# Kernel optimization log

Measured on AMD Instinct MI355X. Metric: run time of the kernel, lower is better.

Reference implementation:

```python
import jax, jax.numpy as jnp
import numpy as np

DIM = 256
HEADS = 8
WS = 7
MLP_HIDDEN = int(DIM * 2.0)
LN_EPS = 1e-5


def _ln(x, g, b):
    m = x.mean(-1, keepdims=True)
    v = ((x - m) ** 2).mean(-1, keepdims=True)
    return (x - m) / jnp.sqrt(v + LN_EPS) * g + b


def setup_inputs() -> dict:
    key = jax.random.key(0)
    ks = jax.random.split(key, 6)
    B, H, W, C = 32, 56, 56, DIM
    s = lambda k, shape: jax.random.normal(k, shape, jnp.float32) * 0.02
    return {
        "x": jax.random.normal(ks[0], (B, H * W, C), jnp.float32),
        "H": H,
        "W": W,
        "norm1_g": jnp.ones((C,), jnp.float32),
        "norm1_b": jnp.zeros((C,), jnp.float32),
        "in_proj_w": s(ks[1], (3 * C, C)),
        "in_proj_b": jnp.zeros((3 * C,), jnp.float32),
        "out_proj_w": s(ks[2], (C, C)),
        "out_proj_b": jnp.zeros((C,), jnp.float32),
        "norm2_g": jnp.ones((C,), jnp.float32),
        "norm2_b": jnp.zeros((C,), jnp.float32),
        "mlp_w1": s(ks[3], (MLP_HIDDEN, C)),
        "mlp_b1": jnp.zeros((MLP_HIDDEN,), jnp.float32),
        "mlp_w2": s(ks[4], (C, MLP_HIDDEN)),
        "mlp_b2": jnp.zeros((C,), jnp.float32),
    }


def reference(x, H, W, norm1_g, norm1_b, in_proj_w, in_proj_b, out_proj_w,
              out_proj_b, norm2_g, norm2_b, mlp_w1, mlp_b1, mlp_w2, mlp_b2):
    B, N, C = x.shape
    ws = WS
    shortcut = x

    h = _ln(x, norm1_g, norm1_b).reshape(B, H, W, C)  # channels-last (equiv. math)
    pad_h = (ws - H % ws) % ws
    pad_w = (ws - W % ws) % ws
    h = jnp.pad(h, ((0, 0), (0, pad_h), (0, pad_w), (0, 0)), mode="reflect")
    Hp, Wp = H + pad_h, W + pad_w
    nh, nw = Hp // ws, Wp // ws

    # window partition -> (B*nh*nw, ws*ws, C)
    h = h.reshape(B, nh, ws, nw, ws, C).transpose(0, 1, 3, 2, 4, 5)
    h = h.reshape(B * nh * nw, ws * ws, C)

    # torch nn.MultiheadAttention (batch_first), q=k=v=h
    hd = C // HEADS
    qkv = h @ in_proj_w.T + in_proj_b               # (Bw, L, 3C)
    q, k, v = jnp.split(qkv, 3, axis=-1)
    Bw, L, _ = q.shape
    q = q.reshape(Bw, L, HEADS, hd).transpose(0, 2, 1, 3)
    k = k.reshape(Bw, L, HEADS, hd).transpose(0, 2, 1, 3)
    v = v.reshape(Bw, L, HEADS, hd).transpose(0, 2, 1, 3)
    scores = jnp.einsum("bhqd,bhkd->bhqk", q, k) / jnp.sqrt(jnp.float32(hd))
    attn = jax.nn.softmax(scores, axis=-1)
    o = jnp.einsum("bhqk,bhkd->bhqd", attn, v)
    o = o.transpose(0, 2, 1, 3).reshape(Bw, L, C)
    o = o @ out_proj_w.T + out_proj_b

    # window merge, crop padding
    o = o.reshape(B, nh, nw, ws, ws, C).transpose(0, 1, 3, 2, 4, 5)
    o = o.reshape(B, Hp, Wp, C)[:, :H, :W, :].reshape(B, N, C)

    x = shortcut + o
    h2 = _ln(x, norm2_g, norm2_b)
    h2 = jax.nn.gelu(h2 @ mlp_w1.T + mlp_b1, approximate=False) @ mlp_w2.T + mlp_b2
    return x + h2
```

## Files before the change

### kernel.cpp

```cpp
#include <hip/hip_runtime.h>
#include <hip/hip_bf16.h>
#include <math.h>

#define NTOK 3136
#define C_ 256
#define HEADS_ 8
#define HD 32
#define WS_ 7
#define L_ 49
#define NWIN 2048
#define NWH 16384
#define M_ 100352
#define MP 131072
#define PLANE 33554432
#define MLPH 512

typedef __bf16 bf16x8 __attribute__((ext_vector_type(8)));
typedef float f32x4 __attribute__((ext_vector_type(4)));

#define VMWAIT(n) asm volatile("s_waitcnt vmcnt(" #n ")" ::: "memory")
#define LGKWAIT   asm volatile("s_waitcnt lgkmcnt(0)" ::: "memory")
#define SBAR      __builtin_amdgcn_s_barrier()

__device__ __forceinline__ unsigned short f2bf(float f) {
    union { float f; unsigned u; } v; v.f = f;
    unsigned r = v.u + 0x7fffu + ((v.u >> 16) & 1u);
    return (unsigned short)(r >> 16);
}
__device__ __forceinline__ float bf2f(unsigned short s) {
    union { unsigned u; float f; } v; v.u = ((unsigned)s) << 16;
    return v.f;
}

__device__ __forceinline__ int t2rr(int t) {
    int win = t / L_;
    int l   = t - win * L_;
    int b_  = win >> 6, wh = (win >> 3) & 7, ww = win & 7;
    int ld7 = l / WS_;
    int y   = wh * WS_ + ld7;
    int xc  = ww * WS_ + (l - ld7 * WS_);
    return b_ * NTOK + y * 56 + xc;
}

template <int NBN>
__device__ __forceinline__ void xcd_decode(int nb, int& bm, int& bn) {
    int h = blockIdx.x;
    int fid = (h & 7) * (nb >> 3) + (h >> 3);
    int bmi = fid / NBN;
    bm = bmi * 128;
    bn = (fid - bmi * NBN) * 128;
}

__global__ __launch_bounds__(256) void cvt_kernel(
    const float* __restrict__ in, unsigned short* __restrict__ out, int n)
{
    int i = blockIdx.x * 256 + threadIdx.x;
    if (i < n) out[i] = f2bf(in[i]);
}

__global__ __launch_bounds__(256) void ln_kernel(
    const float* __restrict__ x, const float* __restrict__ gamma,
    const float* __restrict__ beta, unsigned short* __restrict__ out)
{
    int wave = threadIdx.x >> 6;
    int lane = threadIdx.x & 63;
    int p = blockIdx.x * 4 + wave;
    int win = p >> 6, l = p & 63;
    if (l >= L_) {
        uint2 z; z.x = 0; z.y = 0;
        *(uint2*)(out + (size_t)p * C_ + lane * 4) = z;
        return;
    }
    int b_ = win >> 6, wh = (win >> 3) & 7, ww = win & 7;
    int ld7 = l / WS_;
    int y   = wh * WS_ + ld7;
    int xc  = ww * WS_ + (l - ld7 * WS_);
    int rr  = b_ * NTOK + y * 56 + xc;
    const float* row = x + (size_t)rr * C_;
    float4 v = *(const float4*)(row + lane * 4);
    float s  = v.x + v.y + v.z + v.w;
    float ss = v.x * v.x + v.y * v.y + v.z * v.z + v.w * v.w;
    #pragma unroll
    for (int m = 1; m < 64; m <<= 1) {
        s  += __shfl_xor(s, m, 64);
        ss += __shfl_xor(ss, m, 64);
    }
    float mean = s * (1.0f / C_);
    float var  = ss * (1.0f / C_) - mean * mean;
    float inv  = rsqrtf(var + 1e-5f);
    float4 gv = *(const float4*)(gamma + lane * 4);
    float4 bv = *(const float4*)(beta + lane * 4);
    unsigned short o[4];
    o[0] = f2bf((v.x - mean) * inv * gv.x + bv.x);
    o[1] = f2bf((v.y - mean) * inv * gv.y + bv.y);
    o[2] = f2bf((v.z - mean) * inv * gv.z + bv.z);
    o[3] = f2bf((v.w - mean) * inv * gv.w + bv.w);
    *(uint2*)(out + (size_t)p * C_ + lane * 4) = *(const uint2*)o;
}

#define GBK 32

__device__ __forceinline__ void gload_lds16(const void* g, void* l) {
    __builtin_amdgcn_global_load_lds(
        (const __attribute__((address_space(1))) unsigned*)g,
        (__attribute__((address_space(3))) unsigned*)l, 16, 0, 0);
}

#define TSS 136

__global__ __launch_bounds__(256) void mgemm_qkv(
    const unsigned short* __restrict__ A, const unsigned short* __restrict__ W,
    const float* __restrict__ bias, unsigned short* __restrict__ Qp,
    unsigned short* __restrict__ Kp, unsigned short* __restrict__ Vp)
{
    __shared__ __align__(16) unsigned short pool[16384];
    unsigned short* As0 = pool;
    unsigned short* As1 = pool + 4096;
    unsigned short* Bs0 = pool + 8192;
    unsigned short* Bs1 = pool + 12288;
    unsigned short* Ts  = pool;

    int tid  = threadIdx.x;
    int w    = tid >> 6;
    int lane = tid & 63;
    int wr = w >> 1, wc = w & 1;
    int bm, bn;
    xcd_decode<6>(gridDim.x, bm, bn);
    int srow = lane >> 2;
    int scol = ((lane & 3) ^ ((lane >> 3) & 3)) * 8;
    int c = lane & 15, hi = lane >> 4;
    int hs = (hi ^ ((c >> 1) & 3)) * 8;

    f32x4 acc[4][4] = {};

    auto stage = [&](unsigned short* asd, unsigned short* bsd, int k0) {
        #pragma unroll
        for (int i = 0; i < 2; ++i) {
            int ra = w * 32 + i * 16;
            gload_lds16(A + (size_t)(bm + ra + srow) * 256 + k0 + scol, asd + ra * GBK);
            gload_lds16(W + (size_t)(bn + ra + srow) * 256 + k0 + scol, bsd + ra * GBK);
        }
    };

    stage(As0, Bs0, 0);
    stage(As1, Bs1, GBK);
    VMWAIT(4); SBAR;
    #pragma unroll
    for (int t = 0; t < 8; ++t) {
        unsigned short* as = (t & 1) ? As1 : As0;
        unsigned short* bs = (t & 1) ? Bs1 : Bs0;
        bf16x8 af[4], bf[4];
        #pragma unroll
        for (int mi = 0; mi < 4; ++mi)
            af[mi] = *(const bf16x8*)&as[(wr * 64 + mi * 16 + c) * GBK + hs];
        #pragma unroll
        for (int ni = 0; ni < 4; ++ni)
            bf[ni] = *(const bf16x8*)&bs[(wc * 64 + ni * 16 + c) * GBK + hs];
        LGKWAIT; SBAR;
        if (t + 2 < 8) stage(as, bs, (t + 2) * GBK);
        #pragma unroll
        for (int mi = 0; mi < 4; ++mi)
            #pragma unroll
            for (int ni = 0; ni < 4; ++ni)
                acc[mi][ni] = __builtin_amdgcn_mfma_f32_16x16x32_bf16(
                    af[mi], bf[ni], acc[mi][ni], 0, 0, 0);
        if (t < 7) {
            if (t + 2 < 8) { VMWAIT(4); } else { VMWAIT(0); }
            SBAR;
        }
    }
    __syncthreads();

    int which  = bn >> 8;
    int bn_off = bn & 255;
    unsigned short* plane = (which == 0) ? Qp : (which == 1) ? Kp : Vp;

    #pragma unroll
    for (int ch = 0; ch < 2; ++ch) {
        if (wr == ch) {
            #pragma unroll
            for (int mi = 0; mi < 4; ++mi)
                #pragma unroll
                for (int ni = 0; ni < 4; ++ni) {
                    int colb = wc * 64 + ni * 16 + c;
                    float bv = bias[bn + colb];
                    #pragma unroll
                    for (int r = 0; r < 4; ++r)
                        Ts[(mi * 16 + hi * 4 + r) * TSS + colb] =
                            f2bf(acc[mi][ni][r] + bv);
                }
        }
        __syncthreads();
        int win = (bm >> 6) + ch;
        if (which < 2) {
            #pragma unroll
            for (int it = 0; it < 4; ++it) {
                int id = it * 256 + tid;
                int row = id >> 4, cx = (id & 15) * 8;
                if (row < L_) {
                    uint4 v = *(const uint4*)&Ts[row * TSS + cx];
                    *(uint4*)&plane[(size_t)win * 16384 + (size_t)row * 256 + bn_off + cx] = v;
                }
            }
        } else {
            #pragma unroll
            for (int it = 0; it < 4; ++it) {
                int id = it * 256 + tid;
                int kb = id >> 7, colloc = id & 127;
                union { unsigned short s[8]; uint4 v; } u;
                #pragma unroll
                for (int kj = 0; kj < 8; ++kj)
                    u.s[kj] = Ts[(kb * 8 + kj) * TSS + colloc];
                *(uint4*)&plane[(size_t)win * 16384 +
                                (size_t)(kb * 256 + bn_off + colloc) * 8] = u.v;
            }
        }
        __syncthreads();
    }
}

__global__ __launch_bounds__(256) void mgemm_g(
    const unsigned short* __restrict__ A, const unsigned short* __restrict__ W,
    const float* __restrict__ bias, unsigned short* __restrict__ outp)
{
    __shared__ __align__(16) unsigned short pool[16384];
    unsigned short* As0 = pool;
    unsigned short* As1 = pool + 4096;
    unsigned short* Bs0 = pool + 8192;
    unsigned short* Bs1 = pool + 12288;
    unsigned short* Ts  = pool;

    int tid  = threadIdx.x;
    int w    = tid >> 6;
    int lane = tid & 63;
    int wr = w >> 1, wc = w & 1;
    int bm, bn;
    xcd_decode<4>(gridDim.x, bm, bn);
    int srow = lane >> 2;
    int scol = ((lane & 3) ^ ((lane >> 3) & 3)) * 8;
    int c = lane & 15, hi = lane >> 4;
    int hs = (hi ^ ((c >> 1) & 3)) * 8;

    f32x4 acc[4][4] = {};

    auto stage = [&](unsigned short* asd, unsigned short* bsd, int k0) {
        #pragma unroll
        for (int i = 0; i < 2; ++i) {
            int ra = w * 32 + i * 16;
            gload_lds16(A + (size_t)(bm + ra + srow) * 256 + k0 + scol, asd + ra * GBK);
            gload_lds16(W + (size_t)(bn + ra + srow) * 256 + k0 + scol, bsd + ra * GBK);
        }
    };

    stage(As0, Bs0, 0);
    stage(As1, Bs1, GBK);
    VMWAIT(4); SBAR;
    #pragma unroll
    for (int t = 0; t < 8; ++t) {
        unsigned short* as = (t & 1) ? As1 : As0;
        unsigned short* bs = (t & 1) ? Bs1 : Bs0;
        bf16x8 af[4], bf[4];
        #pragma unroll
        for (int mi = 0; mi < 4; ++mi)
            af[mi] = *(const bf16x8*)&as[(wr * 64 + mi * 16 + c) * GBK + hs];
        #pragma unroll
        for (int ni = 0; ni < 4; ++ni)
            bf[ni] = *(const bf16x8*)&bs[(wc * 64 + ni * 16 + c) * GBK + hs];
        LGKWAIT; SBAR;
        if (t + 2 < 8) stage(as, bs, (t + 2) * GBK);
        #pragma unroll
        for (int mi = 0; mi < 4; ++mi)
            #pragma unroll
            for (int ni = 0; ni < 4; ++ni)
                acc[mi][ni] = __builtin_amdgcn_mfma_f32_16x16x32_bf16(
                    af[mi], bf[ni], acc[mi][ni], 0, 0, 0);
        if (t < 7) {
            if (t + 2 < 8) { VMWAIT(4); } else { VMWAIT(0); }
            SBAR;
        }
    }
    __syncthreads();

    #pragma unroll
    for (int ch = 0; ch < 2; ++ch) {
        if (wr == ch) {
            #pragma unroll
            for (int mi = 0; mi < 4; ++mi)
                #pragma unroll
                for (int ni = 0; ni < 4; ++ni) {
                    int colb = wc * 64 + ni * 16 + c;
                    float bv = bias[bn + colb];
                    #pragma unroll
                    for (int r = 0; r < 4; ++r) {
                        float v = acc[mi][ni][r] + bv;
                        float a = 1.5957691216f * (v + 0.044715f * v * v * v);
                        float g = v / (1.0f + __expf(-a));
                        Ts[(mi * 16 + hi * 4 + r) * TSS + colb] = f2bf(g);
                    }
                }
        }
        __syncthreads();
        #pragma unroll
        for (int it = 0; it < 4; ++it) {
            int id = it * 256 + tid;
            int row = id >> 4, cx = (id & 15) * 8;
            uint4 v = *(const uint4*)&Ts[row * TSS + cx];
            *(uint4*)&outp[(size_t)(bm + ch * 64 + row) * MLPH + bn + cx] = v;
        }
        __syncthreads();
    }
}

#define XS 260

__global__ __launch_bounds__(512) void mgemm_ln(
    const unsigned short* __restrict__ A, const unsigned short* __restrict__ W,
    const float* __restrict__ bias, const float* __restrict__ x,
    const float* __restrict__ g2, const float* __restrict__ b2,
    unsigned short* __restrict__ x1_out, unsigned short* __restrict__ ln_out)
{
    __shared__ __align__(16) unsigned short pool[128 * XS];
    unsigned short* As0 = pool;
    unsigned short* As1 = pool + 4096;
    unsigned short* Bs0 = pool + 8192;
    unsigned short* Bs1 = pool + 16384;

    int tid  = threadIdx.x;
    int w    = tid >> 6;
    int lane = tid & 63;
    int wr = w >> 2, wc = w & 3;
    int bm = blockIdx.x * 128;
    int srow = lane >> 2;
    int scol = ((lane & 3) ^ ((lane >> 3) & 3)) * 8;
    int c = lane & 15, hi = lane >> 4;
    int hs = (hi ^ ((c >> 1) & 3)) * 8;

    f32x4 acc[4][4] = {};

    auto stage = [&](unsigned short* asd, unsigned short* bsd, int k0) {
        gload_lds16(A + (size_t)(bm + w * 16 + srow) * 256 + k0 + scol,
                    asd + (w * 16) * GBK);
        #pragma unroll
        for (int i = 0; i < 2; ++i) {
            int ra = w * 32 + i * 16;
            gload_lds16(W + (size_t)(ra + srow) * 256 + k0 + scol, bsd + ra * GBK);
        }
    };

    stage(As0, Bs0, 0);
    stage(As1, Bs1, GBK);
    VMWAIT(3); SBAR;
    #pragma unroll
    for (int t = 0; t < 8; ++t) {
        unsigned short* as = (t & 1) ? As1 : As0;
        unsigned short* bs = (t & 1) ? Bs1 : Bs0;
        bf16x8 af[4], bf[4];
        #pragma unroll
        for (int mi = 0; mi < 4; ++mi)
            af[mi] = *(const bf16x8*)&as[(wr * 64 + mi * 16 + c) * GBK + hs];
        #pragma unroll
        for (int ni = 0; ni < 4; ++ni)
            bf[ni] = *(const bf16x8*)&bs[(wc * 64 + ni * 16 + c) * GBK + hs];
        LGKWAIT; SBAR;
        if (t + 2 < 8) stage(as, bs, (t + 2) * GBK);
        #pragma unroll
        for (int mi = 0; mi < 4; ++mi)
            #pragma unroll
            for (int ni = 0; ni < 4; ++ni)
                acc[mi][ni] = __builtin_amdgcn_mfma_f32_16x16x32_bf16(
                    af[mi], bf[ni], acc[mi][ni], 0, 0, 0);
        if (t < 7) {
            if (t + 2 < 8) { VMWAIT(3); } else { VMWAIT(0); }
            SBAR;
        }
    }
    __syncthreads();

    #pragma unroll
    for (int mi = 0; mi < 4; ++mi) {
        #pragma unroll
        for (int ni = 0; ni < 4; ++ni) {
            int colb = wc * 64 + ni * 16 + c;
            float bv = bias[colb];
            #pragma unroll
            for (int r = 0; r < 4; ++r)
                pool[(wr * 64 + mi * 16 + hi * 4 + r) * XS + colb] =
                    f2bf(acc[mi][ni][r] + bv);
        }
    }
    __syncthreads();

    float4 gv  = *(const float4*)(g2 + lane * 4);
    float4 bv2 = *(const float4*)(b2 + lane * 4);
    #pragma unroll 2
    for (int i = 0; i < 16; ++i) {
        int tl = w * 16 + i;
        int t = bm + tl;
        int rr = t2rr(t);
        float4 xv = *(const float4*)(x + (size_t)rr * C_ + lane * 4);
        uint2 ov = *(const uint2*)&pool[tl * XS + lane * 4];
        float x0 = xv.x + bf2f(ov.x & 0xffff);
        float x1 = xv.y + bf2f(ov.x >> 16);
        float x2 = xv.z + bf2f(ov.y & 0xffff);
        float x3 = xv.w + bf2f(ov.y >> 16);
        float s  = x0 + x1 + x2 + x3;
        float ss = x0 * x0 + x1 * x1 + x2 * x2 + x3 * x3;
        #pragma unroll
        for (int m = 1; m < 64; m <<= 1) {
            s  += __shfl_xor(s, m, 64);
            ss += __shfl_xor(ss, m, 64);
        }
        float mean = s * (1.0f / C_);
        float var  = ss * (1.0f / C_) - mean * mean;
        float inv  = rsqrtf(var + 1e-5f);
        uint2 xw, lw;
        xw.x = (unsigned)f2bf(x0) | ((unsigned)f2bf(x1) << 16);
        xw.y = (unsigned)f2bf(x2) | ((unsigned)f2bf(x3) << 16);
        float l0 = (x0 - mean) * inv * gv.x + bv2.x;
        float l1 = (x1 - mean) * inv * gv.y + bv2.y;
        float l2 = (x2 - mean) * inv * gv.z + bv2.z;
        float l3 = (x3 - mean) * inv * gv.w + bv2.w;
        lw.x = (unsigned)f2bf(l0) | ((unsigned)f2bf(l1) << 16);
        lw.y = (unsigned)f2bf(l2) | ((unsigned)f2bf(l3) << 16);
        *(uint2*)(x1_out + (size_t)t * C_ + lane * 4) = xw;
        *(uint2*)(ln_out + (size_t)t * C_ + lane * 4) = lw;
    }
}

__global__ __launch_bounds__(256) void mgemm_out(
    const unsigned short* __restrict__ A, const unsigned short* __restrict__ W,
    const float* __restrict__ bias, const unsigned short* __restrict__ x1,
    float* __restrict__ dout)
{
    __shared__ __align__(16) unsigned short pool[16896];
    unsigned short* As0 = pool;
    unsigned short* As1 = pool + 4096;
    unsigned short* Bs0 = pool + 8192;
    unsigned short* Bs1 = pool + 12288;
    float* stg = (float*)pool;

    int tid  = threadIdx.x;
    int w    = tid >> 6;
    int lane = tid & 63;
    int wr = w >> 1, wc = w & 1;
    int bm, bn;
    xcd_decode<2>(gridDim.x, bm, bn);
    int srow = lane >> 2;
    int scol = ((lane & 3) ^ ((lane >> 3) & 3)) * 8;
    int c = lane & 15, hi = lane >> 4;
    int hs = (hi ^ ((c >> 1) & 3)) * 8;

    f32x4 acc[4][4] = {};

    auto stage = [&](unsigned short* asd, unsigned short* bsd, int k0) {
        #pragma unroll
        for (int i = 0; i < 2; ++i) {
            int ra = w * 32 + i * 16;
            gload_lds16(A + (size_t)(bm + ra + srow) * 512 + k0 + scol, asd + ra * GBK);
            gload_lds16(W + (size_t)(bn + ra + srow) * 512 + k0 + scol, bsd + ra * GBK);
        }
    };

    stage(As0, Bs0, 0);
    stage(As1, Bs1, GBK);
    VMWAIT(4); SBAR;
    #pragma unroll
    for (int t = 0; t < 16; ++t) {
        unsigned short* as = (t & 1) ? As1 : As0;
        unsigned short* bs = (t & 1) ? Bs1 : Bs0;
        bf16x8 af[4], bf[4];
        #pragma unroll
        for (int mi = 0; mi < 4; ++mi)
            af[mi] = *(const bf16x8*)&as[(wr * 64 + mi * 16 + c) * GBK + hs];
        #pragma unroll
        for (int ni = 0; ni < 4; ++ni)
            bf[ni] = *(const bf16x8*)&bs[(wc * 64 + ni * 16 + c) * GBK + hs];
        LGKWAIT; SBAR;
        if (t + 2 < 16) stage(as, bs, (t + 2) * GBK);
        #pragma unroll
        for (int mi = 0; mi < 4; ++mi)
            #pragma unroll
            for (int ni = 0; ni < 4; ++ni)
                acc[mi][ni] = __builtin_amdgcn_mfma_f32_16x16x32_bf16(
                    af[mi], bf[ni], acc[mi][ni], 0, 0, 0);
        if (t < 15) {
            if (t + 2 < 16) { VMWAIT(4); } else { VMWAIT(0); }
            SBAR;
        }
    }
    __syncthreads();

    #pragma unroll
    for (int c2 = 0; c2 < 4; ++c2) {
        if (wr == (c2 >> 1)) {
            int mi0 = (c2 & 1) * 2;
            #pragma unroll
            for (int mm = 0; mm < 2; ++mm) {
                #pragma unroll
                for (int ni = 0; ni < 4; ++ni) {
                    int colb = wc * 64 + ni * 16 + c;
                    float bv = bias[bn + colb];
                    #pragma unroll
                    for (int r = 0; r < 4; ++r)
                        stg[(mm * 16 + hi * 4 + r) * 132 + colb] =
                            acc[mi0 + mm][ni][r] + bv;
                }
            }
        }
        __syncthreads();
        #pragma unroll
        for (int i = 0; i < 4; ++i) {
            int lr = i * 8 + (tid >> 5);
            int t = bm + c2 * 32 + lr;
            int rr = t2rr(t);
            int col4 = (tid & 31) * 4;
            float4 v = *(const float4*)&stg[lr * 132 + col4];
            uint2 rv = *(const uint2*)&x1[(size_t)t * C_ + bn + col4];
            v.x += bf2f(rv.x & 0xffff);
            v.y += bf2f(rv.x >> 16);
            v.z += bf2f(rv.y & 0xffff);
            v.w += bf2f(rv.y >> 16);
            *(float4*)&dout[(size_t)rr * C_ + bn + col4] = v;
        }
        __syncthreads();
    }
}

__global__ __launch_bounds__(256) void mattn(
    const unsigned short* __restrict__ Qp, const unsigned short* __restrict__ Kp,
    const unsigned short* __restrict__ Vp, unsigned short* __restrict__ o_win)
{
    __shared__ __align__(16) unsigned short P_lds[4][64][72];
    int wave = threadIdx.x >> 6, lane = threadIdx.x & 63;
    int c = lane & 15, hi = lane >> 4;
    int wh = blockIdx.x * 4 + wave;
    int win = wh >> 3, head = wh & 7;
    const unsigned short* qb = Qp + (size_t)win * 16384 + head * HD;
    const unsigned short* kb = Kp + (size_t)win * 16384 + head * HD;
    const unsigned short* vb = Vp + (size_t)win * 16384 + head * HD * 8;

    bf16x8 af[4], bk[4];
    #pragma unroll
    for (int mi = 0; mi < 4; ++mi)
        af[mi] = *(const bf16x8*)(qb + (size_t)(mi * 16 + c) * 256 + hi * 8);
    #pragma unroll
    for (int ni = 0; ni < 4; ++ni)
        bk[ni] = *(const bf16x8*)(kb + (size_t)(ni * 16 + c) * 256 + hi * 8);

    f32x4 sacc[4][4] = {};
    #pragma unroll
    for (int mi = 0; mi < 4; ++mi)
        #pragma unroll
        for (int ni = 0; ni < 4; ++ni)
            sacc[mi][ni] = __builtin_amdgcn_mfma_f32_16x16x32_bf16(
                af[mi], bk[ni], sacc[mi][ni], 0, 0, 0);

    const float scale = 0.17677669529663687f;
    float inv_[4][4];
    #pragma unroll
    for (int mi = 0; mi < 4; ++mi) {
        #pragma unroll
        for (int r = 0; r < 4; ++r) {
            float sv[4];
            float m = -1e30f;
            #pragma unroll
            for (int ni = 0; ni < 4; ++ni) {
                float v = sacc[mi][ni][r] * scale;
                v = (ni * 16 + c < L_) ? v : -1e30f;
                sv[ni] = v;
                m = fmaxf(m, v);
            }
            #pragma unroll
            for (int msk = 1; msk < 16; msk <<= 1)
                m = fmaxf(m, __shfl_xor(m, msk, 64));
            float sum = 0.f;
            unsigned short pb[4];
            #pragma unroll
            for (int ni = 0; ni < 4; ++ni) {
                float p = __expf(sv[ni] - m);
                sum += p;
                pb[ni] = f2bf(p);
            }
            #pragma unroll
            for (int msk = 1; msk < 16; msk <<= 1)
                sum += __shfl_xor(sum, msk, 64);
            inv_[mi][r] = 1.0f / sum;
            int q = mi * 16 + hi * 4 + r;
            #pragma unroll
            for (int ni = 0; ni < 4; ++ni)
                P_lds[wave][q][ni * 16 + c] = pb[ni];
        }
    }

    f32x4 oacc[4][2] = {};
    #pragma unroll
    for (int ks = 0; ks < 2; ++ks) {
        bf16x8 pa[4], bv[2];
        #pragma unroll
        for (int mi = 0; mi < 4; ++mi)
            pa[mi] = *(const bf16x8*)&P_lds[wave][mi * 16 + c][ks * 32 + hi * 8];
        #pragma unroll
        for (int ni = 0; ni < 2; ++ni)
            bv[ni] = *(const bf16x8*)(vb + (size_t)((ks * 4 + hi) * 256 + ni * 16 + c) * 8);
        #pragma unroll
        for (int mi = 0; mi < 4; ++mi)
            #pragma unroll
            for (int ni = 0; ni < 2; ++ni)
                oacc[mi][ni] = __builtin_amdgcn_mfma_f32_16x16x32_bf16(
                    pa[mi], bv[ni], oacc[mi][ni], 0, 0, 0);
    }

    #pragma unroll
    for (int mi = 0; mi < 4; ++mi) {
        #pragma unroll
        for (int r = 0; r < 4; ++r) {
            int q = mi * 16 + hi * 4 + r;
            if (q < L_) {
                size_t rowoff = ((size_t)(win * L_ + q)) * C_ + head * HD;
                float iv = inv_[mi][r];
                #pragma unroll
                for (int ni = 0; ni < 2; ++ni)
                    o_win[rowoff + ni * 16 + c] = f2bf(oacc[mi][ni][r] * iv);
            }
        }
    }
}

extern "C" void kernel_launch(void* const* d_in, const int* in_sizes, int n_in,
                              void* d_out, int out_size, void* d_ws, size_t ws_size,
                              hipStream_t stream)
{
    (void)in_sizes; (void)n_in; (void)out_size; (void)ws_size;
    const float* x    = (const float*)d_in[0];
    const float* n1g  = (const float*)d_in[3];
    const float* n1b  = (const float*)d_in[4];
    const float* wqkv = (const float*)d_in[5];
    const float* bqkv = (const float*)d_in[6];
    const float* wout = (const float*)d_in[7];
    const float* bout = (const float*)d_in[8];
    const float* n2g  = (const float*)d_in[9];
    const float* n2b  = (const float*)d_in[10];
    const float* w1   = (const float*)d_in[11];
    const float* b1   = (const float*)d_in[12];
    const float* w2   = (const float*)d_in[13];
    const float* b2   = (const float*)d_in[14];
    float* out = (float*)d_out;

    unsigned short* lnq   = (unsigned short*)d_ws;
    unsigned short* Qp    = lnq + (size_t)MP * C_;
    unsigned short* Kp    = Qp + (size_t)PLANE;
    unsigned short* Vp    = Kp + (size_t)PLANE;
    unsigned short* o_win = Vp + (size_t)PLANE;
    unsigned short* wqkv_bf = o_win + (size_t)M_ * C_;
    unsigned short* wout_bf = wqkv_bf + 768 * 256;
    unsigned short* w1_bf   = wout_bf + 256 * 256;
    unsigned short* w2_bf   = w1_bf + 512 * 256;
    unsigned short* x1_bf  = lnq;
    unsigned short* ln2_bf = Vp;
    unsigned short* gelu   = Qp;

    cvt_kernel<<<(768 * 256 + 255) / 256, 256, 0, stream>>>(wqkv, wqkv_bf, 768 * 256);
    cvt_kernel<<<(256 * 256 + 255) / 256, 256, 0, stream>>>(wout, wout_bf, 256 * 256);
    cvt_kernel<<<(512 * 256 + 255) / 256, 256, 0, stream>>>(w1, w1_bf, 512 * 256);
    cvt_kernel<<<(256 * 512 + 255) / 256, 256, 0, stream>>>(w2, w2_bf, 256 * 512);

    ln_kernel<<<MP / 4, 256, 0, stream>>>(x, n1g, n1b, lnq);

    mgemm_qkv<<<(MP / 128) * 6, 256, 0, stream>>>(
        lnq, wqkv_bf, bqkv, Qp, Kp, Vp);

    mattn<<<NWH / 4, 256, 0, stream>>>(Qp, Kp, Vp, o_win);

    mgemm_ln<<<M_ / 128, 512, 0, stream>>>(
        o_win, wout_bf, bout, x, n2g, n2b, x1_bf, ln2_bf);

    mgemm_g<<<(M_ / 128) * 4, 256, 0, stream>>>(ln2_bf, w1_bf, b1, gelu);

    mgemm_out<<<(M_ / 128) * 2, 256, 0, stream>>>(gelu, w2_bf, b2, x1_bf, out);
}
```

Measured before the change: 439.8 us.

## Fuse QKV projection and window attention into one per-window kernel

Replaces the separate QKV GEMM and attention kernels with one kernel that runs one block per 7x7 window. The block computes Q, K and V for its 64 padded rows into a 128KB LDS pool and then runs all eight heads from LDS. This removes the round trip of the three large Q/K/V planes through global memory. In exchange each block reloads the full 768x256 weight matrix for only 64 rows, and the large LDS allocation limits occupancy. The workspace layout is also rearranged because the planes are no longer aliased.

```diff
diff --git a/kernel.cpp b/kernel.cpp
--- a/kernel.cpp
+++ b/kernel.cpp
@@ -9,10 +9,8 @@
 #define WS_ 7
 #define L_ 49
 #define NWIN 2048
-#define NWH 16384
 #define M_ 100352
 #define MP 131072
-#define PLANE 33554432
 #define MLPH 512
 
 typedef __bf16 bf16x8 __attribute__((ext_vector_type(8)));
@@ -106,208 +104,188 @@
         (__attribute__((address_space(3))) unsigned*)l, 16, 0, 0);
 }
 
-#define TSS 136
-
-__global__ __launch_bounds__(256) void mgemm_qkv(
+__global__ __launch_bounds__(512, 2) void qkattn(
     const unsigned short* __restrict__ A, const unsigned short* __restrict__ W,
-    const float* __restrict__ bias, unsigned short* __restrict__ Qp,
-    unsigned short* __restrict__ Kp, unsigned short* __restrict__ Vp)
+    const float* __restrict__ bias, unsigned short* __restrict__ o_win)
 {
-    __shared__ __align__(16) unsigned short pool[16384];
-    unsigned short* As0 = pool;
-    unsigned short* As1 = pool + 4096;
-    unsigned short* Bs0 = pool + 8192;
-    unsigned short* Bs1 = pool + 12288;
-    unsigned short* Ts  = pool;
+    __shared__ __align__(16) unsigned short pool[65536];
 
     int tid  = threadIdx.x;
     int w    = tid >> 6;
     int lane = tid & 63;
-    int wr = w >> 1, wc = w & 1;
-    int bm, bn;
-    xcd_decode<6>(gridDim.x, bm, bn);
+    int c = lane & 15, hi = lane >> 4;
+    int win = blockIdx.x;
+    const unsigned short* Ag = A + (size_t)win * 16384;
+
+    #pragma unroll
+    for (int it = 0; it < 4; ++it) {
+        int idx = it * 512 + tid;
+        int row = idx >> 5, p = idx & 31;
+        gload_lds16(Ag + row * 256 + ((p ^ (row & 7)) << 3),
+                    &pool[(it * 512 + w * 64) * 8]);
+    }
+
     int srow = lane >> 2;
     int scol = ((lane & 3) ^ ((lane >> 3) & 3)) * 8;
-    int c = lane & 15, hi = lane >> 4;
-    int hs = (hi ^ ((c >> 1) & 3)) * 8;
-
-    f32x4 acc[4][4] = {};
-
-    auto stage = [&](unsigned short* asd, unsigned short* bsd, int k0) {
-        #pragma unroll
-        for (int i = 0; i < 2; ++i) {
-            int ra = w * 32 + i * 16;
-            gload_lds16(A + (size_t)(bm + ra + srow) * 256 + k0 + scol, asd + ra * GBK);
-            gload_lds16(W + (size_t)(bn + ra + srow) * 256 + k0 + scol, bsd + ra * GBK);
+    auto stageB = [&](int buf, int k0) {
+        #pragma unroll
+        for (int it = 0; it < 6; ++it) {
+            int row = it * 128 + w * 16 + srow;
+            gload_lds16(W + (size_t)row * 256 + k0 + scol,
+                        &pool[buf + (it * 512 + w * 64) * 8]);
         }
     };
 
-    stage(As0, Bs0, 0);
-    stage(As1, Bs1, GBK);
-    VMWAIT(4); SBAR;
+    f32x4 acc[4][6] = {};
+    stageB(16384, 0);
+    stageB(40960, 32);
+    VMWAIT(6); SBAR;
     #pragma unroll
     for (int t = 0; t < 8; ++t) {
-        unsigned short* as = (t & 1) ? As1 : As0;
-        unsigned short* bs = (t & 1) ? Bs1 : Bs0;
-        bf16x8 af[4], bf[4];
-        #pragma unroll
-        for (int mi = 0; mi < 4; ++mi)
-            af[mi] = *(const bf16x8*)&as[(wr * 64 + mi * 16 + c) * GBK + hs];
-        #pragma unroll
-        for (int ni = 0; ni < 4; ++ni)
-            bf[ni] = *(const bf16x8*)&bs[(wc * 64 + ni * 16 + c) * GBK + hs];
+        int buf = (t & 1) ? 40960 : 16384;
+        bf16x8 af[4], bf[6];
+        #pragma unroll
+        for (int mi = 0; mi < 4; ++mi) {
+            int row = mi * 16 + c;
+            af[mi] = *(const bf16x8*)&pool[row * 256 + (((t * 4 + hi) ^ (c & 7)) << 3)];
+        }
+        int hs = (hi ^ ((c >> 1) & 3)) << 3;
+        #pragma unroll
+        for (int ni = 0; ni < 6; ++ni)
+            bf[ni] = *(const bf16x8*)&pool[buf + ((w * 6 + ni) * 16 + c) * GBK + hs];
         LGKWAIT; SBAR;
-        if (t + 2 < 8) stage(as, bs, (t + 2) * GBK);
-        #pragma unroll
-        for (int mi = 0; mi < 4; ++mi)
-            #pragma unroll
-            for (int ni = 0; ni < 4; ++ni)
+        if (t + 2 < 8) stageB(buf, (t + 2) * GBK);
+        #pragma unroll
+        for (int mi = 0; mi < 4; ++mi)
+            #pragma unroll
+            for (int ni = 0; ni < 6; ++ni)
                 acc[mi][ni] = __builtin_amdgcn_mfma_f32_16x16x32_bf16(
                     af[mi], bf[ni], acc[mi][ni], 0, 0, 0);
         if (t < 7) {
-            if (t + 2 < 8) { VMWAIT(4); } else { VMWAIT(0); }
+            if (t + 2 < 8) { VMWAIT(6); } else { VMWAIT(0); }
             SBAR;
         }
     }
     __syncthreads();
 
-    int which  = bn >> 8;
-    int bn_off = bn & 255;
-    unsigned short* plane = (which == 0) ? Qp : (which == 1) ? Kp : Vp;
-
-    #pragma unroll
-    for (int ch = 0; ch < 2; ++ch) {
-        if (wr == ch) {
-            #pragma unroll
-            for (int mi = 0; mi < 4; ++mi)
-                #pragma unroll
-                for (int ni = 0; ni < 4; ++ni) {
-                    int colb = wc * 64 + ni * 16 + c;
-                    float bv = bias[bn + colb];
-                    #pragma unroll
-                    for (int r = 0; r < 4; ++r)
-                        Ts[(mi * 16 + hi * 4 + r) * TSS + colb] =
-                            f2bf(acc[mi][ni][r] + bv);
-                }
-        }
-        __syncthreads();
-        int win = (bm >> 6) + ch;
-        if (which < 2) {
-            #pragma unroll
-            for (int it = 0; it < 4; ++it) {
-                int id = it * 256 + tid;
-                int row = id >> 4, cx = (id & 15) * 8;
-                if (row < L_) {
-                    uint4 v = *(const uint4*)&Ts[row * TSS + cx];
-                    *(uint4*)&plane[(size_t)win * 16384 + (size_t)row * 256 + bn_off + cx] = v;
+    #pragma unroll
+    for (int ni = 0; ni < 6; ++ni) {
+        int fn = w * 6 + ni;
+        int which = fn >> 4;
+        int colp = ((fn & 15) << 4) + c;
+        float bv = bias[(fn << 4) + c];
+        #pragma unroll
+        for (int mi = 0; mi < 4; ++mi) {
+            #pragma unroll
+            for (int r = 0; r < 4; ++r) {
+                int row = mi * 16 + hi * 4 + r;
+                unsigned short val = f2bf(acc[mi][ni][r] + bv);
+                if (which < 2) {
+                    int pos = (colp >> 3) ^ (row & 7);
+                    pool[which * 16384 + row * 256 + pos * 8 + (colp & 7)] = val;
+                } else {
+                    pool[32768 + (((row >> 3) << 8) + colp) * 8 + (row & 7)] = val;
                 }
             }
-        } else {
-            #pragma unroll
-            for (int it = 0; it < 4; ++it) {
-                int id = it * 256 + tid;
-                int kb = id >> 7, colloc = id & 127;
-                union { unsigned short s[8]; uint4 v; } u;
+        }
+    }
+    __syncthreads();
+
+    int h = w;
+    bf16x8 aq[4], bk[4];
+    #pragma unroll
+    for (int mi = 0; mi < 4; ++mi) {
+        int row = mi * 16 + c;
+        int pos8 = ((h * 4 + hi) ^ (c & 7)) << 3;
+        aq[mi] = *(const bf16x8*)&pool[row * 256 + pos8];
+        bk[mi] = *(const bf16x8*)&pool[16384 + row * 256 + pos8];
+    }
+    __syncthreads();
+
+    f32x4 sacc[4][4] = {};
+    #pragma unroll
+    for (int mi = 0; mi < 4; ++mi)
+        #pragma unroll
+        for (int ni = 0; ni < 4; ++ni)
+            sacc[mi][ni] = __builtin_amdgcn_mfma_f32_16x16x32_bf16(
+                aq[mi], bk[ni], sacc[mi][ni], 0, 0, 0);
+
+    const float scale = 0.17677669529663687f;
+    float inv_[4][4];
+    unsigned short* Pb = &pool[h * 4096];
+    #pragma unroll
+    for (int mi = 0; mi < 4; ++mi) {
+        #pragma unroll
+        for (int r = 0; r < 4; ++r) {
+            float sv[4];
+            float m = -1e30f;
+            #pragma unroll
+            for (int ni = 0; ni < 4; ++ni) {
+                float v = sacc[mi][ni][r] * scale;
+                v = (ni * 16 + c < L_) ? v : -1e30f;
+                sv[ni] = v;
+                m = fmaxf(m, v);
+            }
+            #pragma unroll
+            for (int msk = 1; msk < 16; msk <<= 1)
+                m = fmaxf(m, __shfl_xor(m, msk, 64));
+            float sum = 0.f;
+            unsigned short pb[4];
+            #pragma unroll
+            for (int ni = 0; ni < 4; ++ni) {
+                float p = __expf(sv[ni] - m);
+                sum += p;
+                pb[ni] = f2bf(p);
+            }
+            #pragma unroll
+            for (int msk = 1; msk < 16; msk <<= 1)
+                sum += __shfl_xor(sum, msk, 64);
+            inv_[mi][r] = 1.0f / sum;
+            int q = mi * 16 + hi * 4 + r;
+            int qs = q & 7;
+            #pragma unroll
+            for (int ni = 0; ni < 4; ++ni) {
+                int k = ni * 16 + c;
+                int pos = ((k >> 3) ^ qs);
+                Pb[q * 64 + pos * 8 + (k & 7)] = pb[ni];
+            }
+        }
+    }
+
+    f32x4 oacc[4][2] = {};
+    #pragma unroll
+    for (int ks = 0; ks < 2; ++ks) {
+        bf16x8 pa[4], bv[2];
+        #pragma unroll
+        for (int mi = 0; mi < 4; ++mi) {
+            int row = mi * 16 + c;
+            pa[mi] = *(const bf16x8*)&Pb[row * 64 + (((ks * 4 + hi) ^ (c & 7)) << 3)];
+        }
+        #pragma unroll
+        for (int ni = 0; ni < 2; ++ni)
+            bv[ni] = *(const bf16x8*)&pool[32768 +
+                ((ks * 4 + hi) * 256 + h * HD + ni * 16 + c) * 8];
+        #pragma unroll
+        for (int mi = 0; mi < 4; ++mi)
+            #pragma unroll
+            for (int ni = 0; ni < 2; ++ni)
+                oacc[mi][ni] = __builtin_amdgcn_mfma_f32_16x16x32_bf16(
+                    pa[mi], bv[ni], oacc[mi][ni], 0, 0, 0);
+    }
+
+    #pragma unroll
+    for (int mi = 0; mi < 4; ++mi) {
+        #pragma unroll
+        for (int r = 0; r < 4; ++r) {
+            int q = mi * 16 + hi * 4 + r;
+            if (q < L_) {
+                size_t rowoff = ((size_t)(win * L_ + q)) * C_ + h * HD;
+                float iv = inv_[mi][r];
                 #pragma unroll
-                for (int kj = 0; kj < 8; ++kj)
-                    u.s[kj] = Ts[(kb * 8 + kj) * TSS + colloc];
-                *(uint4*)&plane[(size_t)win * 16384 +
-                                (size_t)(kb * 256 + bn_off + colloc) * 8] = u.v;
+                for (int ni = 0; ni < 2; ++ni)
+                    o_win[rowoff + ni * 16 + c] = f2bf(oacc[mi][ni][r] * iv);
             }
         }
-        __syncthreads();
-    }
-}
-
-__global__ __launch_bounds__(256) void mgemm_g(
-    const unsigned short* __restrict__ A, const unsigned short* __restrict__ W,
-    const float* __restrict__ bias, unsigned short* __restrict__ outp)
-{
-    __shared__ __align__(16) unsigned short pool[16384];
-    unsigned short* As0 = pool;
-    unsigned short* As1 = pool + 4096;
-    unsigned short* Bs0 = pool + 8192;
-    unsigned short* Bs1 = pool + 12288;
-    unsigned short* Ts  = pool;
-
-    int tid  = threadIdx.x;
-    int w    = tid >> 6;
-    int lane = tid & 63;
-    int wr = w >> 1, wc = w & 1;
-    int bm, bn;
-    xcd_decode<4>(gridDim.x, bm, bn);
-    int srow = lane >> 2;
-    int scol = ((lane & 3) ^ ((lane >> 3) & 3)) * 8;
-    int c = lane & 15, hi = lane >> 4;
-    int hs = (hi ^ ((c >> 1) & 3)) * 8;
-
-    f32x4 acc[4][4] = {};
-
-    auto stage = [&](unsigned short* asd, unsigned short* bsd, int k0) {
-        #pragma unroll
-        for (int i = 0; i < 2; ++i) {
-            int ra = w * 32 + i * 16;
-            gload_lds16(A + (size_t)(bm + ra + srow) * 256 + k0 + scol, asd + ra * GBK);
-            gload_lds16(W + (size_t)(bn + ra + srow) * 256 + k0 + scol, bsd + ra * GBK);
-        }
-    };
-
-    stage(As0, Bs0, 0);
-    stage(As1, Bs1, GBK);
-    VMWAIT(4); SBAR;
-    #pragma unroll
-    for (int t = 0; t < 8; ++t) {
-        unsigned short* as = (t & 1) ? As1 : As0;
-        unsigned short* bs = (t & 1) ? Bs1 : Bs0;
-        bf16x8 af[4], bf[4];
-        #pragma unroll
-        for (int mi = 0; mi < 4; ++mi)
-            af[mi] = *(const bf16x8*)&as[(wr * 64 + mi * 16 + c) * GBK + hs];
-        #pragma unroll
-        for (int ni = 0; ni < 4; ++ni)
-            bf[ni] = *(const bf16x8*)&bs[(wc * 64 + ni * 16 + c) * GBK + hs];
-        LGKWAIT; SBAR;
-        if (t + 2 < 8) stage(as, bs, (t + 2) * GBK);
-        #pragma unroll
-        for (int mi = 0; mi < 4; ++mi)
-            #pragma unroll
-            for (int ni = 0; ni < 4; ++ni)
-                acc[mi][ni] = __builtin_amdgcn_mfma_f32_16x16x32_bf16(
-                    af[mi], bf[ni], acc[mi][ni], 0, 0, 0);
-        if (t < 7) {
-            if (t + 2 < 8) { VMWAIT(4); } else { VMWAIT(0); }
-            SBAR;
-        }
-    }
-    __syncthreads();
-
-    #pragma unroll
-    for (int ch = 0; ch < 2; ++ch) {
-        if (wr == ch) {
-            #pragma unroll
-            for (int mi = 0; mi < 4; ++mi)
-                #pragma unroll
-                for (int ni = 0; ni < 4; ++ni) {
-                    int colb = wc * 64 + ni * 16 + c;
-                    float bv = bias[bn + colb];
-                    #pragma unroll
-                    for (int r = 0; r < 4; ++r) {
-                        float v = acc[mi][ni][r] + bv;
-                        float a = 1.5957691216f * (v + 0.044715f * v * v * v);
-                        float g = v / (1.0f + __expf(-a));
-                        Ts[(mi * 16 + hi * 4 + r) * TSS + colb] = f2bf(g);
-                    }
-                }
-        }
-        __syncthreads();
-        #pragma unroll
-        for (int it = 0; it < 4; ++it) {
-            int id = it * 256 + tid;
-            int row = id >> 4, cx = (id & 15) * 8;
-            uint4 v = *(const uint4*)&Ts[row * TSS + cx];
-            *(uint4*)&outp[(size_t)(bm + ch * 64 + row) * MLPH + bn + cx] = v;
-        }
-        __syncthreads();
     }
 }
 
@@ -427,6 +405,100 @@
     }
 }
 
+#define TSS 136
+
+__global__ __launch_bounds__(256) void mgemm_g(
+    const unsigned short* __restrict__ A, const unsigned short* __restrict__ W,
+    const float* __restrict__ bias, unsigned short* __restrict__ outp)
+{
+    __shared__ __align__(16) unsigned short pool[16384];
+    unsigned short* As0 = pool;
+    unsigned short* As1 = pool + 4096;
+    unsigned short* Bs0 = pool + 8192;
+    unsigned short* Bs1 = pool + 12288;
+    unsigned short* Ts  = pool;
+
+    int tid  = threadIdx.x;
+    int w    = tid >> 6;
+    int lane = tid & 63;
+    int wr = w >> 1, wc = w & 1;
+    int bm, bn;
+    xcd_decode<4>(gridDim.x, bm, bn);
+    int srow = lane >> 2;
+    int scol = ((lane & 3) ^ ((lane >> 3) & 3)) * 8;
+    int c = lane & 15, hi = lane >> 4;
+    int hs = (hi ^ ((c >> 1) & 3)) * 8;
+
+    f32x4 acc[4][4] = {};
+
+    auto stage = [&](unsigned short* asd, unsigned short* bsd, int k0) {
+        #pragma unroll
+        for (int i = 0; i < 2; ++i) {
+            int ra = w * 32 + i * 16;
+            gload_lds16(A + (size_t)(bm + ra + srow) * 256 + k0 + scol, asd + ra * GBK);
+            gload_lds16(W + (size_t)(bn + ra + srow) * 256 + k0 + scol, bsd + ra * GBK);
+        }
+    };
+
+    stage(As0, Bs0, 0);
+    stage(As1, Bs1, GBK);
+    VMWAIT(4); SBAR;
+    #pragma unroll
+    for (int t = 0; t < 8; ++t) {
+        unsigned short* as = (t & 1) ? As1 : As0;
+        unsigned short* bs = (t & 1) ? Bs1 : Bs0;
+        bf16x8 af[4], bf[4];
+        #pragma unroll
+        for (int mi = 0; mi < 4; ++mi)
+            af[mi] = *(const bf16x8*)&as[(wr * 64 + mi * 16 + c) * GBK + hs];
+        #pragma unroll
+        for (int ni = 0; ni < 4; ++ni)
+            bf[ni] = *(const bf16x8*)&bs[(wc * 64 + ni * 16 + c) * GBK + hs];
+        LGKWAIT; SBAR;
+        if (t + 2 < 8) stage(as, bs, (t + 2) * GBK);
+        #pragma unroll
+        for (int mi = 0; mi < 4; ++mi)
+            #pragma unroll
+            for (int ni = 0; ni < 4; ++ni)
+                acc[mi][ni] = __builtin_amdgcn_mfma_f32_16x16x32_bf16(
+                    af[mi], bf[ni], acc[mi][ni], 0, 0, 0);
+        if (t < 7) {
+            if (t + 2 < 8) { VMWAIT(4); } else { VMWAIT(0); }
+            SBAR;
+        }
+    }
+    __syncthreads();
+
+    #pragma unroll
+    for (int ch = 0; ch < 2; ++ch) {
+        if (wr == ch) {
+            #pragma unroll
+            for (int mi = 0; mi < 4; ++mi)
+                #pragma unroll
+                for (int ni = 0; ni < 4; ++ni) {
+                    int colb = wc * 64 + ni * 16 + c;
+                    float bv = bias[bn + colb];
+                    #pragma unroll
+                    for (int r = 0; r < 4; ++r) {
+                        float v = acc[mi][ni][r] + bv;
+                        float a = 1.5957691216f * (v + 0.044715f * v * v * v);
+                        float g = v / (1.0f + __expf(-a));
+                        Ts[(mi * 16 + hi * 4 + r) * TSS + colb] = f2bf(g);
+                    }
+                }
+        }
+        __syncthreads();
+        #pragma unroll
+        for (int it = 0; it < 4; ++it) {
+            int id = it * 256 + tid;
+            int row = id >> 4, cx = (id & 15) * 8;
+            uint4 v = *(const uint4*)&Ts[row * TSS + cx];
+            *(uint4*)&outp[(size_t)(bm + ch * 64 + row) * MLPH + bn + cx] = v;
+        }
+        __syncthreads();
+    }
+}
+
 __global__ __launch_bounds__(256) void mgemm_out(
     const unsigned short* __restrict__ A, const unsigned short* __restrict__ W,
     const float* __restrict__ bias, const unsigned short* __restrict__ x1,
@@ -523,106 +595,6 @@
             *(float4*)&dout[(size_t)rr * C_ + bn + col4] = v;
         }
         __syncthreads();
-    }
-}
-
-__global__ __launch_bounds__(256) void mattn(
-    const unsigned short* __restrict__ Qp, const unsigned short* __restrict__ Kp,
-    const unsigned short* __restrict__ Vp, unsigned short* __restrict__ o_win)
-{
-    __shared__ __align__(16) unsigned short P_lds[4][64][72];
-    int wave = threadIdx.x >> 6, lane = threadIdx.x & 63;
-    int c = lane & 15, hi = lane >> 4;
-    int wh = blockIdx.x * 4 + wave;
-    int win = wh >> 3, head = wh & 7;
-    const unsigned short* qb = Qp + (size_t)win * 16384 + head * HD;
-    const unsigned short* kb = Kp + (size_t)win * 16384 + head * HD;
-    const unsigned short* vb = Vp + (size_t)win * 16384 + head * HD * 8;
-
-    bf16x8 af[4], bk[4];
-    #pragma unroll
-    for (int mi = 0; mi < 4; ++mi)
-        af[mi] = *(const bf16x8*)(qb + (size_t)(mi * 16 + c) * 256 + hi * 8);
-    #pragma unroll
-    for (int ni = 0; ni < 4; ++ni)
-        bk[ni] = *(const bf16x8*)(kb + (size_t)(ni * 16 + c) * 256 + hi * 8);
-
-    f32x4 sacc[4][4] = {};
-    #pragma unroll
-    for (int mi = 0; mi < 4; ++mi)
-        #pragma unroll
-        for (int ni = 0; ni < 4; ++ni)
-            sacc[mi][ni] = __builtin_amdgcn_mfma_f32_16x16x32_bf16(
-                af[mi], bk[ni], sacc[mi][ni], 0, 0, 0);
-
-    const float scale = 0.17677669529663687f;
-    float inv_[4][4];
-    #pragma unroll
-    for (int mi = 0; mi < 4; ++mi) {
-        #pragma unroll
-        for (int r = 0; r < 4; ++r) {
-            float sv[4];
-            float m = -1e30f;
-            #pragma unroll
-            for (int ni = 0; ni < 4; ++ni) {
-                float v = sacc[mi][ni][r] * scale;
-                v = (ni * 16 + c < L_) ? v : -1e30f;
-                sv[ni] = v;
-                m = fmaxf(m, v);
-            }
-            #pragma unroll
-            for (int msk = 1; msk < 16; msk <<= 1)
-                m = fmaxf(m, __shfl_xor(m, msk, 64));
-            float sum = 0.f;
-            unsigned short pb[4];
-            #pragma unroll
-            for (int ni = 0; ni < 4; ++ni) {
-                float p = __expf(sv[ni] - m);
-                sum += p;
-                pb[ni] = f2bf(p);
-            }
-            #pragma unroll
-            for (int msk = 1; msk < 16; msk <<= 1)
-                sum += __shfl_xor(sum, msk, 64);
-            inv_[mi][r] = 1.0f / sum;
-            int q = mi * 16 + hi * 4 + r;
-            #pragma unroll
-            for (int ni = 0; ni < 4; ++ni)
-                P_lds[wave][q][ni * 16 + c] = pb[ni];
-        }
-    }
-
-    f32x4 oacc[4][2] = {};
-    #pragma unroll
-    for (int ks = 0; ks < 2; ++ks) {
-        bf16x8 pa[4], bv[2];
-        #pragma unroll
-        for (int mi = 0; mi < 4; ++mi)
-            pa[mi] = *(const bf16x8*)&P_lds[wave][mi * 16 + c][ks * 32 + hi * 8];
-        #pragma unroll
-        for (int ni = 0; ni < 2; ++ni)
-            bv[ni] = *(const bf16x8*)(vb + (size_t)((ks * 4 + hi) * 256 + ni * 16 + c) * 8);
-        #pragma unroll
-        for (int mi = 0; mi < 4; ++mi)
-            #pragma unroll
-            for (int ni = 0; ni < 2; ++ni)
-                oacc[mi][ni] = __builtin_amdgcn_mfma_f32_16x16x32_bf16(
-                    pa[mi], bv[ni], oacc[mi][ni], 0, 0, 0);
-    }
-
-    #pragma unroll
-    for (int mi = 0; mi < 4; ++mi) {
-        #pragma unroll
-        for (int r = 0; r < 4; ++r) {
-            int q = mi * 16 + hi * 4 + r;
-            if (q < L_) {
-                size_t rowoff = ((size_t)(win * L_ + q)) * C_ + head * HD;
-                float iv = inv_[mi][r];
-                #pragma unroll
-                for (int ni = 0; ni < 2; ++ni)
-                    o_win[rowoff + ni * 16 + c] = f2bf(oacc[mi][ni][r] * iv);
-            }
-        }
     }
 }
 
@@ -646,18 +618,15 @@
     const float* b2   = (const float*)d_in[14];
     float* out = (float*)d_out;
 
-    unsigned short* lnq   = (unsigned short*)d_ws;
-    unsigned short* Qp    = lnq + (size_t)MP * C_;
-    unsigned short* Kp    = Qp + (size_t)PLANE;
-    unsigned short* Vp    = Kp + (size_t)PLANE;
-    unsigned short* o_win = Vp + (size_t)PLANE;
-    unsigned short* wqkv_bf = o_win + (size_t)M_ * C_;
+    unsigned short* lnq    = (unsigned short*)d_ws;
+    unsigned short* o_win  = lnq + (size_t)MP * C_;
+    unsigned short* x1_bf  = o_win + (size_t)M_ * C_;
+    unsigned short* ln2_bf = x1_bf + (size_t)M_ * C_;
+    unsigned short* gelu   = ln2_bf + (size_t)M_ * C_;
+    unsigned short* wqkv_bf = gelu + (size_t)M_ * MLPH;
     unsigned short* wout_bf = wqkv_bf + 768 * 256;
     unsigned short* w1_bf   = wout_bf + 256 * 256;
     unsigned short* w2_bf   = w1_bf + 512 * 256;
-    unsigned short* x1_bf  = lnq;
-    unsigned short* ln2_bf = Vp;
-    unsigned short* gelu   = Qp;
 
     cvt_kernel<<<(768 * 256 + 255) / 256, 256, 0, stream>>>(wqkv, wqkv_bf, 768 * 256);
     cvt_kernel<<<(256 * 256 + 255) / 256, 256, 0, stream>>>(wout, wout_bf, 256 * 256);
@@ -666,10 +635,7 @@
 
     ln_kernel<<<MP / 4, 256, 0, stream>>>(x, n1g, n1b, lnq);
 
-    mgemm_qkv<<<(MP / 128) * 6, 256, 0, stream>>>(
-        lnq, wqkv_bf, bqkv, Qp, Kp, Vp);
-
-    mattn<<<NWH / 4, 256, 0, stream>>>(Qp, Kp, Vp, o_win);
+    qkattn<<<NWIN, 512, 0, stream>>>(lnq, wqkv_bf, bqkv, o_win);
 
     mgemm_ln<<<M_ / 128, 512, 0, stream>>>(
         o_win, wout_bf, bout, x, n2g, n2b, x1_bf, ln2_bf);
```

Result: no change. 448.1 us (+1.9%).
